# Optimization experiments

Measured on AMD Instinct MI355X. Metric: run time of the kernel, lower is better.

Reference implementation:

```python
import jax, jax.numpy as jnp
import numpy as np

N, E, D, H, C = 50000, 800000, 64, 2, 64  # nodes, edges, feat, heads, per-head out


def _transformer_conv(x, src, dst, wq, bq, wk, bk, wv, bv, ws, bs):
    n = x.shape[0]
    q = (x @ wq + bq).reshape(n, H, C)
    k = (x @ wk + bk).reshape(n, H, C)
    v = (x @ wv + bv).reshape(n, H, C)
    qi = q[dst]           # [E,H,C] gather at target nodes
    kj = k[src]           # [E,H,C] gather at source nodes
    vj = v[src]
    alpha = jnp.einsum('ehc,ehc->eh', qi, kj) / jnp.sqrt(jnp.asarray(C, x.dtype))
    # segment softmax over incoming edges of each dst node
    amax = jax.ops.segment_max(alpha, dst, num_segments=n)          # [N,H]
    amax = jnp.where(jnp.isfinite(amax), amax, 0.0)
    ex = jnp.exp(alpha - amax[dst])                                  # [E,H]
    denom = jax.ops.segment_sum(ex, dst, num_segments=n)            # [N,H]
    a = ex / (denom[dst] + 1e-16)
    out = jax.ops.segment_sum(a[:, :, None] * vj, dst, num_segments=n)  # [N,H,C]
    out = out.mean(axis=1)                                           # concat=False -> mean heads
    return out + x @ ws + bs                                         # root (skip) connection


def setup_inputs() -> dict:
    key = jax.random.key(0)
    ks = jax.random.split(key, 20)
    x = jax.random.normal(ks[0], (N, D), dtype=jnp.float32)
    edge_index = jax.random.randint(ks[1], (2, E), 0, N, dtype=jnp.int64)
    s = 1.0 / np.sqrt(D)
    def lin(k, din, dout):
        return jax.random.uniform(k, (din, dout), jnp.float32, -s, s)
    inp = {"x": x, "edge_index": edge_index}
    i = 2
    for l, din in ((1, D), (2, C)):
        for nm, dout in (("wq", H * C), ("wk", H * C), ("wv", H * C), ("ws", C)):
            inp[f"l{l}_{nm}"] = lin(ks[i], din, dout); i += 1
            inp[f"l{l}_{nm.replace('w','b')}"] = jnp.zeros((dout,), jnp.float32)
    return inp


def reference(x, edge_index,
              l1_wq, l1_bq, l1_wk, l1_bk, l1_wv, l1_bv, l1_ws, l1_bs,
              l2_wq, l2_bq, l2_wk, l2_bk, l2_wv, l2_bv, l2_ws, l2_bs):
    src, dst = edge_index[0], edge_index[1]
    h = _transformer_conv(x, src, dst, l1_wq, l1_bq, l1_wk, l1_bk, l1_wv, l1_bv, l1_ws, l1_bs)
    h = _transformer_conv(h, src, dst, l2_wq, l2_bq, l2_wk, l2_bk, l2_wv, l2_bv, l2_ws, l2_bs)
    return h
```

## Files before the change

kernel.cpp:

```cpp
#include <hip/hip_runtime.h>
#include <hip/hip_fp16.h>
#include <math.h>


typedef _Float16 half8 __attribute__((ext_vector_type(8)));
typedef _Float16 half4 __attribute__((ext_vector_type(4)));
typedef float floatx4 __attribute__((ext_vector_type(4)));

struct __align__(16) H8 { __half2 a, b, c, d; };
struct __align__(16) F16x8 { _Float16 v[8]; };

static __device__ inline __half2 shfl_xor_h2(__half2 v, int off) {
    union { __half2 h; int i; } u;
    u.h = v;
    u.i = __shfl_xor(u.i, off);
    return u.h;
}

__global__ __launch_bounds__(256) void prep_w_both(
    const float* __restrict__ W0, const float* __restrict__ B0,
    const float* __restrict__ W1, const float* __restrict__ B1,
    const float* __restrict__ W2, const float* __restrict__ B2,
    const float* __restrict__ W3, const float* __restrict__ B3,
    const float* __restrict__ W4, const float* __restrict__ B4,
    const float* __restrict__ W5, const float* __restrict__ B5,
    const float* __restrict__ W6, const float* __restrict__ B6,
    const float* __restrict__ W7, const float* __restrict__ B7,
    _Float16* __restrict__ wht1, _Float16* __restrict__ wht2,
    float* __restrict__ ball1, float* __restrict__ ball2,
    int* __restrict__ counts, int* __restrict__ gcounter, int n) {
    const int tid = blockIdx.x * 256 + threadIdx.x;
    const int nt  = gridDim.x * 256;
    for (int idx = tid; idx < 448 * 64; idx += nt) {
        int c = idx >> 6, k = idx & 63;
        float v1, v2;
        if (c < 128)      { v1 = W0[k*128 + c];       v2 = W4[k*128 + c]; }
        else if (c < 256) { v1 = W1[k*128 + (c-128)]; v2 = W5[k*128 + (c-128)]; }
        else if (c < 384) { v1 = W2[k*128 + (c-256)]; v2 = W6[k*128 + (c-256)]; }
        else              { v1 = W3[k*64 + (c-384)];  v2 = W7[k*64 + (c-384)]; }
        wht1[c*64 + k] = (_Float16)v1;
        wht2[c*64 + k] = (_Float16)v2;
        if (k == 0) {
            float b1, b2;
            if (c < 128)      { b1 = B0[c];     b2 = B4[c]; }
            else if (c < 256) { b1 = B1[c-128]; b2 = B5[c-128]; }
            else if (c < 384) { b1 = B2[c-256]; b2 = B6[c-256]; }
            else              { b1 = B3[c-384]; b2 = B7[c-384]; }
            ball1[c] = b1;
            ball2[c] = b2;
        }
    }
    for (int i = tid; i < n; i += nt) counts[i] = 0;
    if (tid == 0) *gcounter = 0;
}

template <int F32IN>
static __device__ __forceinline__ void gemm_tile_body(
    const void* __restrict__ Xin, int rows,
    const _Float16* __restrict__ WhT, const float* __restrict__ Ball,
    _Float16* __restrict__ Qo, _Float16* __restrict__ KVo,
    float* __restrict__ So, int blk, int tix) {
    const int lane = tix & 63;
    const int w    = tix >> 6;
    const int kg   = lane >> 4;
    const int li   = lane & 15;
    const int rbase = blk * 64 + w * 16;
    const int row  = rbase + li;
    const int crow = row < rows ? row : rows - 1;

    half8 a0, a1;
    if constexpr (F32IN) {
        const float* xp = (const float*)Xin + (size_t)crow * 64 + kg * 8;
        float4 f0 = *(const float4*)xp;
        float4 f1 = *(const float4*)(xp + 4);
        float4 f2 = *(const float4*)(xp + 32);
        float4 f3 = *(const float4*)(xp + 36);
        a0 = half8{(_Float16)f0.x, (_Float16)f0.y, (_Float16)f0.z, (_Float16)f0.w,
                   (_Float16)f1.x, (_Float16)f1.y, (_Float16)f1.z, (_Float16)f1.w};
        a1 = half8{(_Float16)f2.x, (_Float16)f2.y, (_Float16)f2.z, (_Float16)f2.w,
                   (_Float16)f3.x, (_Float16)f3.y, (_Float16)f3.z, (_Float16)f3.w};
    } else {
        const _Float16* xp = (const _Float16*)Xin + (size_t)crow * 64 + kg * 8;
        a0 = *(const half8*)xp;
        a1 = *(const half8*)(xp + 32);
    }

#pragma unroll
    for (int t = 0; t < 28; ++t) {
        const _Float16* wp = WhT + (size_t)(t * 16 + li) * 64 + kg * 8;
        half8 b0 = *(const half8*)wp;
        half8 b1 = *(const half8*)(wp + 32);
        floatx4 acc = {0.f, 0.f, 0.f, 0.f};
        acc = __builtin_amdgcn_mfma_f32_16x16x32_f16(b0, a0, acc, 0, 0, 0);
        acc = __builtin_amdgcn_mfma_f32_16x16x32_f16(b1, a1, acc, 0, 0, 0);
        const int c0 = t * 16 + kg * 4;
        float4 bias = *(const float4*)(Ball + c0);
        if (row < rows) {
            float o0 = acc[0] + bias.x, o1 = acc[1] + bias.y;
            float o2 = acc[2] + bias.z, o3 = acc[3] + bias.w;
            if (t < 8) {
                *(half4*)(Qo + (size_t)row * 128 + c0) =
                    half4{(_Float16)o0, (_Float16)o1, (_Float16)o2, (_Float16)o3};
            } else if (t < 24) {
                *(half4*)(KVo + (size_t)row * 256 + (c0 - 128)) =
                    half4{(_Float16)o0, (_Float16)o1, (_Float16)o2, (_Float16)o3};
            } else {
                *(float4*)(So + (size_t)row * 64 + (c0 - 384)) =
                    make_float4(o0, o1, o2, o3);
            }
        }
    }
}

__global__ __launch_bounds__(256) void gemm1_hist(
    const float* __restrict__ X, int rows,
    const _Float16* __restrict__ WhT, const float* __restrict__ Ball,
    _Float16* __restrict__ Qo, _Float16* __restrict__ KVo,
    float* __restrict__ So,
    const int* __restrict__ dst, int* __restrict__ counts, int e, int gb) {
    if ((int)blockIdx.x < gb) {
        gemm_tile_body<1>(X, rows, WhT, Ball, Qo, KVo, So,
                          blockIdx.x, threadIdx.x);
    } else {
        int i = ((int)blockIdx.x - gb) * 256 + threadIdx.x;
        if (i < e) atomicAdd(&counts[dst[i]], 1);
    }
}

__global__ __launch_bounds__(256) void alloc_kernel(
    const int* __restrict__ counts, int* __restrict__ gcounter,
    int* __restrict__ offsets, int* __restrict__ cursor, int n) {
    int idx = blockIdx.x * 256 + threadIdx.x;
    int lane = threadIdx.x & 63;
    int v = (idx < n) ? counts[idx] : 0;
    int pre = v;
#pragma unroll
    for (int off = 1; off < 64; off <<= 1) {
        int u = __shfl_up(pre, off);
        if (lane >= off) pre += u;
    }
    int wtot = __shfl(pre, 63);
    int base = 0;
    if (lane == 63) base = atomicAdd(gcounter, wtot);
    base = __shfl(base, 63);
    if (idx < n) {
        int ex = base + pre - v;
        offsets[idx] = ex;
        cursor[idx]  = ex;
    }
}

__global__ __launch_bounds__(256) void scatter_kernel(const int* __restrict__ src,
                                                      const int* __restrict__ dst,
                                                      int* __restrict__ cursor,
                                                      int* __restrict__ ssrc, int e) {
    int i = blockIdx.x * 256 + threadIdx.x;
    if (i < e) {
        int pos = atomicAdd(&cursor[dst[i]], 1);
        ssrc[pos] = src[i];
    }
}

template <int F32IN>
__global__ __launch_bounds__(256) void gemm_mfma(
    const void* __restrict__ Xin, int rows,
    const _Float16* __restrict__ WhT, const float* __restrict__ Ball,
    _Float16* __restrict__ Qo, _Float16* __restrict__ KVo,
    float* __restrict__ So) {
    gemm_tile_body<F32IN>(Xin, rows, WhT, Ball, Qo, KVo, So,
                          blockIdx.x, threadIdx.x);
}

template <int HALF_OUT>
__global__ __launch_bounds__(256) void attn_kernel(
    const _Float16* __restrict__ Qh,
    const _Float16* __restrict__ KV,
    const int* __restrict__ offs, const int* __restrict__ cnts,
    const int* __restrict__ ssrc,
    const float* __restrict__ skip,
    float* __restrict__ outF, _Float16* __restrict__ outH, int n) {
    int node = (blockIdx.x * 256 + threadIdx.x) >> 6;
    int lane = threadIdx.x & 63;
    if (node >= n) return;
    const int slot = lane >> 4;
    const int koff = ((lane >> 3) & 1) * 64 + (lane & 7) * 8;

    H8 q = *(const H8*)(Qh + (size_t)node * 128 + koff);

    const int beg = offs[node];
    const int end = beg + cnts[node];
    float m = -INFINITY, l = 0.f;
    __half2 hz = __float2half2_rn(0.f);
    __half2 ha = hz, hb = hz, hc = hz, hd = hz;

    int i = beg;
    bool b0 = false, b1 = false;
    H8 k0, k1, v0, v1;
    if (i < end) {
        int e0 = i + slot, e1 = i + 4 + slot;
        b0 = e0 < end; b1 = e1 < end;
        int s0 = ssrc[b0 ? e0 : end - 1];
        int s1 = ssrc[b1 ? e1 : end - 1];
        const _Float16* p0 = KV + (size_t)s0 * 256 + koff;
        const _Float16* p1 = KV + (size_t)s1 * 256 + koff;
        k0 = *(const H8*)p0; v0 = *(const H8*)(p0 + 128);
        k1 = *(const H8*)p1; v1 = *(const H8*)(p1 + 128);
    }

    while (i < end) {
        const int inext = i + 8;
        bool nb0 = false, nb1 = false;
        H8 nk0, nk1, nv0, nv1;
        if (inext < end) {
            int e0 = inext + slot, e1 = inext + 4 + slot;
            nb0 = e0 < end; nb1 = e1 < end;
            int s0 = ssrc[nb0 ? e0 : end - 1];
            int s1 = ssrc[nb1 ? e1 : end - 1];
            const _Float16* p0 = KV + (size_t)s0 * 256 + koff;
            const _Float16* p1 = KV + (size_t)s1 * 256 + koff;
            nk0 = *(const H8*)p0; nv0 = *(const H8*)(p0 + 128);
            nk1 = *(const H8*)p1; nv1 = *(const H8*)(p1 + 128);
        }

        __half2 dh0 = __hfma2(q.a, k0.a, __hfma2(q.b, k0.b, __hfma2(q.c, k0.c, __hmul2(q.d, k0.d))));
        __half2 dh1 = __hfma2(q.a, k1.a, __hfma2(q.b, k1.b, __hfma2(q.c, k1.c, __hmul2(q.d, k1.d))));
        __half2 pd = __halves2half2(__hadd(dh0.x, dh0.y), __hadd(dh1.x, dh1.y));
        pd = __hadd2(pd, shfl_xor_h2(pd, 1));
        pd = __hadd2(pd, shfl_xor_h2(pd, 2));
        pd = __hadd2(pd, shfl_xor_h2(pd, 4));
        float d0 = b0 ? __half2float(pd.x) * 0.125f : -INFINITY;
        float d1 = b1 ? __half2float(pd.y) * 0.125f : -INFINITY;

        float mx = fmaxf(fmaxf(d0, d1), m);
        float sc = (m == -INFINITY) ? 0.f : __expf(m - mx);
        float p0e = b0 ? __expf(d0 - mx) : 0.f;
        float p1e = b1 ? __expf(d1 - mx) : 0.f;
        l = fmaf(l, sc, p0e + p1e);

        __half2 hsc = __float2half2_rn(sc);
        __half2 hp0 = __float2half2_rn(p0e);
        __half2 hp1 = __float2half2_rn(p1e);
        ha = __hfma2(hp0, v0.a, __hfma2(hp1, v1.a, __hmul2(ha, hsc)));
        hb = __hfma2(hp0, v0.b, __hfma2(hp1, v1.b, __hmul2(hb, hsc)));
        hc = __hfma2(hp0, v0.c, __hfma2(hp1, v1.c, __hmul2(hc, hsc)));
        hd = __hfma2(hp0, v0.d, __hfma2(hp1, v1.d, __hmul2(hd, hsc)));
        m = mx;

        i = inext;
        b0 = nb0; b1 = nb1;
        k0 = nk0; k1 = nk1; v0 = nv0; v1 = nv1;
    }

    float acc[8];
    {
        float2 t0 = __half22float2(ha), t1 = __half22float2(hb);
        float2 t2 = __half22float2(hc), t3 = __half22float2(hd);
        acc[0] = t0.x; acc[1] = t0.y; acc[2] = t1.x; acc[3] = t1.y;
        acc[4] = t2.x; acc[5] = t2.y; acc[6] = t3.x; acc[7] = t3.y;
    }

#pragma unroll
    for (int off = 16; off <= 32; off <<= 1) {
        float mo = __shfl_xor(m, off);
        float lo = __shfl_xor(l, off);
        float ao[8];
#pragma unroll
        for (int j = 0; j < 8; ++j) ao[j] = __shfl_xor(acc[j], off);
        float mm = fmaxf(m, mo);
        float sa = (m  == -INFINITY) ? 0.f : __expf(m  - mm);
        float sb = (mo == -INFINITY) ? 0.f : __expf(mo - mm);
        l = l * sa + lo * sb;
#pragma unroll
        for (int j = 0; j < 8; ++j) acc[j] = acc[j] * sa + ao[j] * sb;
        m = mm;
    }
    float inv = 1.f / (l + 1e-16f);
    float r[8];
#pragma unroll
    for (int j = 0; j < 8; ++j) r[j] = acc[j] * inv;
#pragma unroll
    for (int j = 0; j < 8; ++j) r[j] = 0.5f * (r[j] + __shfl_xor(r[j], 8));

    if (lane < 8) {
        const float4* sp = (const float4*)(skip + (size_t)node * 64 + lane * 8);
        float4 s0 = sp[0], s1 = sp[1];
        float o[8] = {s0.x + r[0], s0.y + r[1], s0.z + r[2], s0.w + r[3],
                      s1.x + r[4], s1.y + r[5], s1.z + r[6], s1.w + r[7]};
        if (HALF_OUT) {
            F16x8 h;
#pragma unroll
            for (int j = 0; j < 8; ++j) h.v[j] = (_Float16)o[j];
            *(F16x8*)(outH + (size_t)node * 64 + lane * 8) = h;
        } else {
            float4* op = (float4*)(outF + (size_t)node * 64 + lane * 8);
            op[0] = make_float4(o[0], o[1], o[2], o[3]);
            op[1] = make_float4(o[4], o[5], o[6], o[7]);
        }
    }
}

extern "C" void kernel_launch(void* const* d_in, const int* in_sizes, int n_in,
                              void* d_out, int out_size, void* d_ws, size_t ws_size,
                              hipStream_t stream) {
    const float* x  = (const float*)d_in[0];
    const int*   ei = (const int*)d_in[1];
    const int N = in_sizes[0] / 64;
    const int E = in_sizes[1] / 2;

    const float* w[16];
    for (int i = 0; i < 16; ++i) w[i] = (const float*)d_in[2 + i];

    char* base = (char*)d_ws;
    size_t off = 0;
    auto alloc = [&](size_t bytes) {
        void* p = base + off;
        off = (off + bytes + 255) & ~(size_t)255;
        return p;
    };
    _Float16* qh   = (_Float16*)alloc((size_t)N * 128 * 2);
    _Float16* kv   = (_Float16*)alloc((size_t)N * 256 * 2);
    float*    sk1  = (float*)alloc((size_t)N * 64 * 4);
    _Float16* h1h  = (_Float16*)alloc((size_t)N * 64 * 2);
    _Float16* wht1 = (_Float16*)alloc(448 * 64 * 2);
    _Float16* wht2 = (_Float16*)alloc(448 * 64 * 2);
    float*    ball1 = (float*)alloc(448 * 4);
    float*    ball2 = (float*)alloc(448 * 4);
    int* counts    = (int*)alloc((size_t)N * 4);
    int* offsets   = (int*)alloc((size_t)(N + 1) * 4);
    int* cursor    = (int*)alloc((size_t)N * 4);
    int* ssrc      = (int*)alloc((size_t)E * 4);
    int* gcounter  = (int*)alloc(256 * 4);

    prep_w_both<<<224, 256, 0, stream>>>(
        w[0], w[1], w[2], w[3], w[4], w[5], w[6], w[7],
        w[8], w[9], w[10], w[11], w[12], w[13], w[14], w[15],
        wht1, wht2, ball1, ball2, counts, gcounter, N);

    const int eb = (E + 255) / 256;
    const int nb = (N + 255) / 256;
    const int gb = (N + 63) / 64;
    const int ab = (N * 64 + 255) / 256;

    gemm1_hist<<<gb + eb, 256, 0, stream>>>(x, N, wht1, ball1, qh, kv, sk1,
                                            ei + E, counts, E, gb);
    alloc_kernel<<<nb, 256, 0, stream>>>(counts, gcounter, offsets, cursor, N);
    scatter_kernel<<<eb, 256, 0, stream>>>(ei, ei + E, cursor, ssrc, E);

    attn_kernel<1><<<ab, 256, 0, stream>>>(qh, kv, offsets, counts, ssrc, sk1,
                                           nullptr, h1h, N);
    gemm_mfma<0><<<gb, 256, 0, stream>>>(h1h, N, wht2, ball2, qh, kv, (float*)d_out);
    attn_kernel<0><<<ab, 256, 0, stream>>>(qh, kv, offsets, counts, ssrc, (float*)d_out,
                                           (float*)d_out, nullptr, N);
}
```

Before: 278.3 us.

## Stage GEMM weights in LDS and split histogram out of fused GEMM kernel

```diff
diff --git a/kernel.cpp b/kernel.cpp
--- a/kernel.cpp
+++ b/kernel.cpp
@@ -55,16 +55,29 @@
 }
 
 template <int F32IN>
-static __device__ __forceinline__ void gemm_tile_body(
+__global__ __launch_bounds__(256) void gemm_mfma(
     const void* __restrict__ Xin, int rows,
-    const _Float16* __restrict__ WhT, const float* __restrict__ Ball,
-    _Float16* __restrict__ Qo, _Float16* __restrict__ KVo,
-    float* __restrict__ So, int blk, int tix) {
+    const _Float16* __restrict__ WhT,
+    const float* __restrict__ Ball,
+    _Float16* __restrict__ Qo,
+    _Float16* __restrict__ KVo,
+    float* __restrict__ So) {
+    __shared__ _Float16 wlds[448 * 72];
+    const int tix = threadIdx.x;
+
+    {
+        const int* wsrc = (const int*)WhT;
+        for (int i = tix; i < 448 * 32; i += 256) {
+            int r = i >> 5, e = (i & 31) * 2;
+            *(int*)&wlds[r * 72 + e] = wsrc[i];
+        }
+    }
+
     const int lane = tix & 63;
     const int w    = tix >> 6;
     const int kg   = lane >> 4;
     const int li   = lane & 15;
-    const int rbase = blk * 64 + w * 16;
+    const int rbase = blockIdx.x * 64 + w * 16;
     const int row  = rbase + li;
     const int crow = row < rows ? row : rows - 1;
 
@@ -84,10 +97,11 @@
         a0 = *(const half8*)xp;
         a1 = *(const half8*)(xp + 32);
     }
+    __syncthreads();
 
 #pragma unroll
     for (int t = 0; t < 28; ++t) {
-        const _Float16* wp = WhT + (size_t)(t * 16 + li) * 64 + kg * 8;
+        const _Float16* wp = &wlds[(t * 16 + li) * 72 + kg * 8];
         half8 b0 = *(const half8*)wp;
         half8 b1 = *(const half8*)(wp + 32);
         floatx4 acc = {0.f, 0.f, 0.f, 0.f};
@@ -112,19 +126,10 @@
     }
 }
 
-__global__ __launch_bounds__(256) void gemm1_hist(
-    const float* __restrict__ X, int rows,
-    const _Float16* __restrict__ WhT, const float* __restrict__ Ball,
-    _Float16* __restrict__ Qo, _Float16* __restrict__ KVo,
-    float* __restrict__ So,
-    const int* __restrict__ dst, int* __restrict__ counts, int e, int gb) {
-    if ((int)blockIdx.x < gb) {
-        gemm_tile_body<1>(X, rows, WhT, Ball, Qo, KVo, So,
-                          blockIdx.x, threadIdx.x);
-    } else {
-        int i = ((int)blockIdx.x - gb) * 256 + threadIdx.x;
-        if (i < e) atomicAdd(&counts[dst[i]], 1);
-    }
+__global__ __launch_bounds__(256) void hist_kernel(const int* __restrict__ dst,
+                                                   int* __restrict__ counts, int e) {
+    int i = blockIdx.x * 256 + threadIdx.x;
+    if (i < e) atomicAdd(&counts[dst[i]], 1);
 }
 
 __global__ __launch_bounds__(256) void alloc_kernel(
@@ -159,16 +164,6 @@
         int pos = atomicAdd(&cursor[dst[i]], 1);
         ssrc[pos] = src[i];
     }
-}
-
-template <int F32IN>
-__global__ __launch_bounds__(256) void gemm_mfma(
-    const void* __restrict__ Xin, int rows,
-    const _Float16* __restrict__ WhT, const float* __restrict__ Ball,
-    _Float16* __restrict__ Qo, _Float16* __restrict__ KVo,
-    float* __restrict__ So) {
-    gemm_tile_body<F32IN>(Xin, rows, WhT, Ball, Qo, KVo, So,
-                          blockIdx.x, threadIdx.x);
 }
 
 template <int HALF_OUT>
@@ -341,8 +336,9 @@
     const int gb = (N + 63) / 64;
     const int ab = (N * 64 + 255) / 256;
 
-    gemm1_hist<<<gb + eb, 256, 0, stream>>>(x, N, wht1, ball1, qh, kv, sk1,
-                                            ei + E, counts, E, gb);
+    gemm_mfma<1><<<gb, 256, 0, stream>>>(x, N, wht1, ball1, qh, kv, sk1);
+
+    hist_kernel<<<eb, 256, 0, stream>>>(ei + E, counts, E);
     alloc_kernel<<<nb, 256, 0, stream>>>(counts, gcounter, offsets, cursor, N);
     scatter_kernel<<<eb, 256, 0, stream>>>(ei, ei + E, cursor, ssrc, E);
 
```

After: 277.0 us. About the same (-0.5%).
